# Kernel tuning notes

Hardware: AMD Instinct MI355X
Metric: run time of the kernel (lower is better)

The kernel has to match this reference:

```python
import jax, jax.numpy as jnp
import numpy as np

B, T, H, V = 32, 16, 768, 32000
EPS = 1e-5


def _conv(x, w, stride, pad):
    return jax.lax.conv_general_dilated(
        x, w, (stride, stride), [(pad, pad), (pad, pad)],
        dimension_numbers=('NCHW', 'OIHW', 'NCHW'))


def _bn(x, g, b, m, v):
    inv = g / jnp.sqrt(v + EPS)
    return x * inv[None, :, None, None] + (b - m * inv)[None, :, None, None]


def setup_inputs() -> dict:
    key = jax.random.key(0)
    ks = iter(jax.random.split(key, 48))

    def rn(shape, s=0.02):
        return s * jax.random.normal(next(ks), shape, jnp.float32)

    def bn_params(c):
        g = 1.0 + 0.1 * jax.random.normal(next(ks), (c,), jnp.float32)
        b = 0.1 * jax.random.normal(next(ks), (c,), jnp.float32)
        m = 0.1 * jax.random.normal(next(ks), (c,), jnp.float32)
        v = jax.random.uniform(next(ks), (c,), jnp.float32, 0.5, 1.5)
        return g, b, m, v

    inp = {}
    inp['images'] = jax.random.normal(next(ks), (B, 3, 224, 224), jnp.float32)
    inp['captions'] = jax.random.randint(next(ks), (B, T), 0, V)

    inp['conv1_w'] = rn((64, 3, 7, 7))
    inp['bn1_g'], inp['bn1_b'], inp['bn1_m'], inp['bn1_v'] = bn_params(64)
    inp['conv2_w'] = rn((128, 64, 3, 3))
    inp['bn2_g'], inp['bn2_b'], inp['bn2_m'], inp['bn2_v'] = bn_params(128)
    inp['conv3_w'] = rn((256, 128, 3, 3))
    inp['bn3_g'], inp['bn3_b'], inp['bn3_m'], inp['bn3_v'] = bn_params(256)
    inp['conv4_w'] = rn((H, 256, 3, 3))
    inp['bn4_g'], inp['bn4_b'], inp['bn4_m'], inp['bn4_v'] = bn_params(H)

    emb = rn((V, H), 1.0)
    inp['emb_table'] = emb.at[0].set(0.0)  # padding_idx=0 row is zero
    inp['attn_w'] = rn((H, H))             # attn_proj (no bias)
    inp['w_ih'] = rn((4 * H, 2 * H))       # LSTM input weights (i,f,g,o)
    inp['w_hh'] = rn((4 * H, H))
    inp['b_ih'] = rn((4 * H,))
    inp['b_hh'] = rn((4 * H,))
    inp['fc_w'] = rn((V, H))
    inp['fc_b'] = rn((V,))
    return inp


def _forward(images, captions, conv1_w, bn1_g, bn1_b, bn1_m, bn1_v,
             conv2_w, bn2_g, bn2_b, bn2_m, bn2_v,
             conv3_w, bn3_g, bn3_b, bn3_m, bn3_v,
             conv4_w, bn4_g, bn4_b, bn4_m, bn4_v,
             emb_table, attn_w, w_ih, w_hh, b_ih, b_hh, fc_w, fc_b):
    # ---- ResNetEncoder ----
    x = jax.nn.relu(_bn(_conv(images, conv1_w, 2, 3), bn1_g, bn1_b, bn1_m, bn1_v))
    x = jax.lax.reduce_window(x, -jnp.inf, jax.lax.max, (1, 1, 3, 3), (1, 1, 2, 2),
                              ((0, 0), (0, 0), (1, 1), (1, 1)))
    x = jax.nn.relu(_bn(_conv(x, conv2_w, 1, 1), bn2_g, bn2_b, bn2_m, bn2_v))
    x = jax.nn.relu(_bn(_conv(x, conv3_w, 2, 1), bn3_g, bn3_b, bn3_m, bn3_v))
    x = jax.nn.relu(_bn(_conv(x, conv4_w, 1, 1), bn4_g, bn4_b, bn4_m, bn4_v))
    b, c, hh, ww = x.shape
    memory = x.reshape(b, c, hh * ww).transpose(0, 2, 1)[:, :196, :]  # [B,196,H]

    # ---- LSTMAttnDecoder ----
    emb = emb_table[captions]  # [B,T,H]
    h0 = jnp.zeros((b, H), jnp.float32)
    c0 = jnp.zeros((b, H), jnp.float32)

    def step(carry, e_t):
        h, cst = carry
        q = h @ attn_w.T                                    # [B,H]
        scores = jnp.einsum('bh,bmh->bm', q, memory)        # [B,196]
        ctx = jnp.einsum('bm,bmh->bh', jax.nn.softmax(scores, axis=-1), memory)
        xin = jnp.concatenate([e_t, ctx], axis=-1)          # [B,2H]
        gates = xin @ w_ih.T + b_ih + h @ w_hh.T + b_hh     # [B,4H]
        i, f, g, o = jnp.split(gates, 4, axis=-1)
        c_new = jax.nn.sigmoid(f) * cst + jax.nn.sigmoid(i) * jnp.tanh(g)
        h_new = jax.nn.sigmoid(o) * jnp.tanh(c_new)
        logits = h_new @ fc_w.T + fc_b                      # [B,V]
        return (h_new, c_new), logits

    (hT, cT), logits = jax.lax.scan(step, (h0, c0), emb.transpose(1, 0, 2))
    logits = logits.transpose(1, 0, 2)  # [B,T,V]
    return logits, (hT[None], cT[None])


def reference(images, captions, conv1_w, bn1_g, bn1_b, bn1_m, bn1_v,
              conv2_w, bn2_g, bn2_b, bn2_m, bn2_v,
              conv3_w, bn3_g, bn3_b, bn3_m, bn3_v,
              conv4_w, bn4_g, bn4_b, bn4_m, bn4_v,
              emb_table, attn_w, w_ih, w_hh, b_ih, b_hh, fc_w, fc_b):
    return _forward(images, captions, conv1_w, bn1_g, bn1_b, bn1_m, bn1_v,
                    conv2_w, bn2_g, bn2_b, bn2_m, bn2_v,
                    conv3_w, bn3_g, bn3_b, bn3_m, bn3_v,
                    conv4_w, bn4_g, bn4_b, bn4_m, bn4_v,
                    emb_table, attn_w, w_ih, w_hh, b_ih, b_hh, fc_w, fc_b)
```

## Files before the change

### kernel.cpp

```cpp
#include <hip/hip_runtime.h>
#include <math.h>

#define NB 32
#define NT 16
#define NH 768
#define NV 32000

typedef short bf16x8 __attribute__((ext_vector_type(8)));
typedef float floatx4 __attribute__((ext_vector_type(4)));
typedef unsigned short ushort_t;

__device__ __forceinline__ float bf2f(unsigned short h) {
    unsigned u = ((unsigned)h) << 16;
    return __builtin_bit_cast(float, u);
}
__device__ __forceinline__ unsigned short f2bf(float f) {
    unsigned u = __builtin_bit_cast(unsigned, f);
    u += 0x7fffu + ((u >> 16) & 1u);
    return (unsigned short)(u >> 16);
}
__device__ __forceinline__ float sigmoidf_(float x) { return 1.f / (1.f + expf(-x)); }

__global__ void bn_prep(const float* __restrict__ g, const float* __restrict__ b,
                        const float* __restrict__ m, const float* __restrict__ v,
                        float* __restrict__ scale, float* __restrict__ bias, int C) {
    int i = blockIdx.x * 256 + threadIdx.x;
    if (i < C) {
        float inv = g[i] * rsqrtf(v[i] + 1e-5f);
        scale[i] = inv;
        bias[i] = b[i] - m[i] * inv;
    }
}

__global__ __launch_bounds__(256) void zfill(unsigned long long* __restrict__ p, long long n) {
    long long i = (long long)blockIdx.x * 256 + threadIdx.x;
    if (i < n) p[i] = 0ULL;
}

__global__ __launch_bounds__(256) void cvt_packW_conv(const float* __restrict__ w, ushort_t* __restrict__ dst,
                                                      int CIN, int total) {
    int idx = blockIdx.x * 256 + threadIdx.x;
    if (idx >= total) return;
    int e = idx & 7, lane = (idx >> 3) & 63, j = (idx >> 9) & 3;
    int r = idx >> 11;
    int KQ = CIN >> 5;
    int kq = r % KQ; r /= KQ;
    int tap = r % 9; int nt = r / 9;
    int co = nt * 64 + j * 16 + (lane & 15);
    int ci = kq * 32 + (lane >> 4) * 8 + e;
    dst[idx] = f2bf(w[((size_t)co * CIN + ci) * 9 + tap]);
}

__global__ __launch_bounds__(256) void cvt_wcombP(const float* __restrict__ w_ih, const float* __restrict__ w_hh,
                                                  ushort_t* __restrict__ dst) {
    int idx = blockIdx.x * 256 + threadIdx.x;
    if (idx >= 3072 * 1536) return;
    int e = idx & 7, lane = (idx >> 3) & 63;
    int t = idx >> 9;
    int kq = t % 48, gg = t / 48;
    int g = gg & 3, bx = gg >> 2;
    int j = g * 768 + bx * 16 + (lane & 15);
    int k = kq * 32 + (lane >> 4) * 8 + e;
    float v = (k < NH) ? w_ih[(size_t)j * (2 * NH) + NH + k] : w_hh[(size_t)j * NH + (k - NH)];
    dst[idx] = f2bf(v);
}

__global__ __launch_bounds__(256) void cvt_wattnTP(const float* __restrict__ w, ushort_t* __restrict__ dst) {
    int idx = blockIdx.x * 256 + threadIdx.x;
    if (idx >= 768 * 768) return;
    int e = idx & 7, lane = (idx >> 3) & 63, j = (idx >> 9) & 3;
    int t = idx >> 11;
    int kq = t % 24, nt = t / 24;
    int n = nt * 64 + 16 * j + (lane & 15);
    int k = kq * 32 + (lane >> 4) * 8 + e;
    dst[idx] = f2bf(w[(size_t)k * 768 + n]);
}

__global__ __launch_bounds__(256) void cvt_pad(const float* __restrict__ src, ushort_t* __restrict__ dst) {
    int idx = blockIdx.x * 256 + threadIdx.x;
    if (idx >= 64 * 160) return;
    int co = idx / 160, k = idx % 160;
    dst[idx] = (k < 147) ? f2bf(src[co * 147 + k]) : (ushort_t)0;
}

__global__ __launch_bounds__(256) void im2col1(const float* __restrict__ img, ushort_t* __restrict__ A) {
    int idx = blockIdx.x * 256 + threadIdx.x;
    const int total = 121856 * 160;
    if (idx >= total) return;
    int k = idx % 160;
    int m = idx / 160;
    ushort_t v = 0;
    if (k < 147) {
        int b = m / 3808;
        int rm = m % 3808;
        int y = rm / 112, x = rm % 112;
        int ci = k / 49;
        int r = k % 49;
        int ky = r / 7, kx = r % 7;
        int iy = 2 * y - 3 + ky;
        int ix = 2 * x - 3 + kx;
        if ((unsigned)iy < 224u && (unsigned)ix < 224u)
            v = f2bf(img[((size_t)(b * 3 + ci) * 224 + iy) * 224 + ix]);
    }
    A[idx] = v;
}

__global__ __launch_bounds__(256) void conv1_gemm(
    const ushort_t* __restrict__ A, const ushort_t* __restrict__ Bw,
    const float* __restrict__ scale, const float* __restrict__ bias,
    ushort_t* __restrict__ out) {
    int lane = threadIdx.x & 63, w = threadIdx.x >> 6;
    int m0 = (blockIdx.x * 4 + w) * 64;
    int lr = lane & 15, kl = (lane >> 4) * 8;
    floatx4 acc[4][4];
    #pragma unroll
    for (int i = 0; i < 4; ++i)
        #pragma unroll
        for (int j = 0; j < 4; ++j) acc[i][j] = 0.f;
    #pragma unroll
    for (int k0 = 0; k0 < 160; k0 += 32) {
        bf16x8 a[4], bb[4];
        #pragma unroll
        for (int i = 0; i < 4; ++i) a[i] = *(const bf16x8*)(A + (size_t)(m0 + 16 * i + lr) * 160 + kl + k0);
        #pragma unroll
        for (int j = 0; j < 4; ++j) bb[j] = *(const bf16x8*)(Bw + (size_t)(16 * j + lr) * 160 + kl + k0);
        #pragma unroll
        for (int i = 0; i < 4; ++i)
            #pragma unroll
            for (int j = 0; j < 4; ++j)
                acc[i][j] = __builtin_amdgcn_mfma_f32_16x16x32_bf16(a[i], bb[j], acc[i][j], 0, 0, 0);
    }
    #pragma unroll
    for (int i = 0; i < 4; ++i) {
        #pragma unroll
        for (int r = 0; r < 4; ++r) {
            int m = m0 + 16 * i + (lane >> 4) * 4 + r;
            int b = m / 3808;
            int rm = m % 3808;
            int y = rm / 112, x = rm % 112;
            #pragma unroll
            for (int j = 0; j < 4; ++j) {
                int n = 16 * j + lr;
                float v = fmaxf(acc[i][j][r] * scale[n] + bias[n], 0.f);
                out[((size_t)(b * 34 + y) * 112 + x) * 64 + n] = f2bf(v);
            }
        }
    }
}

__global__ __launch_bounds__(256) void pool_kernel(const ushort_t* __restrict__ in,
                                                   ushort_t* __restrict__ hal2) {
    int idx = blockIdx.x * 256 + threadIdx.x;
    const int total = 32 * 17 * 56 * 8;
    if (idx >= total) return;
    int c8 = idx & 7;
    int rest = idx >> 3;
    int x = rest % 56; rest /= 56;
    int y = rest % 17; int b = rest / 17;
    float mx[8];
    #pragma unroll
    for (int j = 0; j < 8; ++j) mx[j] = -INFINITY;
    for (int dy = -1; dy <= 1; ++dy) {
        int iy = 2 * y + dy;
        if ((unsigned)iy >= 34u) continue;
        for (int dx = -1; dx <= 1; ++dx) {
            int ix = 2 * x + dx;
            if ((unsigned)ix >= 112u) continue;
            bf16x8 v = *(const bf16x8*)(in + (((size_t)(b * 34 + iy)) * 112 + ix) * 64 + c8 * 8);
            #pragma unroll
            for (int j = 0; j < 8; ++j) mx[j] = fmaxf(mx[j], bf2f((unsigned short)v[j]));
        }
    }
    bf16x8 o;
    #pragma unroll
    for (int j = 0; j < 8; ++j) o[j] = (short)f2bf(mx[j]);
    *(bf16x8*)(hal2 + (((size_t)(b * 19 + y + 1)) * 58 + (x + 1)) * 64 + c8 * 8) = o;
}

template <int CIN, int HH, int WH, int STRIDE, int HOUT, int WOUT, int COUT, int MEMOUT, int OH, int OW>
__global__ __launch_bounds__(64) void conv_mfma(
    const ushort_t* __restrict__ in, const ushort_t* __restrict__ wtP,
    const float* __restrict__ scale, const float* __restrict__ bias,
    ushort_t* __restrict__ out) {
    int lane = threadIdx.x;
    int mt = blockIdx.x, nt = blockIdx.y;
    int lr = lane & 15, kl = (lane >> 4) * 8;
    int rowoff[4];
    #pragma unroll
    for (int i = 0; i < 4; ++i) {
        int m = mt * 64 + 16 * i + lr;
        int b = m / (HOUT * WOUT);
        int rm = m % (HOUT * WOUT);
        int y = rm / WOUT, x = rm % WOUT;
        rowoff[i] = ((b * HH + y * STRIDE) * WH + x * STRIDE) * CIN + kl;
    }
    floatx4 acc[4][4];
    #pragma unroll
    for (int i = 0; i < 4; ++i)
        #pragma unroll
        for (int j = 0; j < 4; ++j) acc[i][j] = 0.f;

    #pragma unroll
    for (int ky = 0; ky < 3; ++ky) {
        #pragma unroll
        for (int kx = 0; kx < 3; ++kx) {
            int ioff = (ky * WH + kx) * CIN;
            int t = ky * 3 + kx;
            #pragma unroll
            for (int k0 = 0; k0 < CIN; k0 += 32) {
                bf16x8 a[4], bb[4];
                #pragma unroll
                for (int i = 0; i < 4; ++i)
                    a[i] = *(const bf16x8*)(in + rowoff[i] + ioff + k0);
                #pragma unroll
                for (int j = 0; j < 4; ++j)
                    bb[j] = *(const bf16x8*)(wtP + ((((size_t)(nt * 9 + t) * (CIN / 32) + (k0 >> 5)) * 4 + j) * 64 + lane) * 8);
                #pragma unroll
                for (int i = 0; i < 4; ++i)
                    #pragma unroll
                    for (int j = 0; j < 4; ++j)
                        acc[i][j] = __builtin_amdgcn_mfma_f32_16x16x32_bf16(a[i], bb[j], acc[i][j], 0, 0, 0);
            }
        }
    }
    #pragma unroll
    for (int i = 0; i < 4; ++i) {
        #pragma unroll
        for (int r = 0; r < 4; ++r) {
            int m = mt * 64 + 16 * i + (lane >> 4) * 4 + r;
            int b = m / (HOUT * WOUT);
            int rm = m % (HOUT * WOUT);
            int y = rm / WOUT, x = rm % WOUT;
            #pragma unroll
            for (int j = 0; j < 4; ++j) {
                int n = nt * 64 + 16 * j + lr;
                float v = fmaxf(acc[i][j][r] * scale[n] + bias[n], 0.f);
                ushort_t hv = f2bf(v);
                if (MEMOUT) {
                    out[(size_t)m * COUT + n] = hv;
                } else {
                    out[((size_t)(b * OH + y + 1) * OW + (x + 1)) * COUT + n] = hv;
                }
            }
        }
    }
}

__global__ __launch_bounds__(64) void kmat_gemm(
    const ushort_t* __restrict__ memv, const ushort_t* __restrict__ Bp,
    ushort_t* __restrict__ KT) {
    int lane = threadIdx.x;
    int mt = blockIdx.x, nt = blockIdx.y;
    int lr = lane & 15, kl = (lane >> 4) * 8;
    floatx4 acc[4][4];
    #pragma unroll
    for (int i = 0; i < 4; ++i)
        #pragma unroll
        for (int j = 0; j < 4; ++j) acc[i][j] = 0.f;
    for (int kq = 0; kq < 24; ++kq) {
        bf16x8 a[4], bb[4];
        #pragma unroll
        for (int i = 0; i < 4; ++i)
            a[i] = *(const bf16x8*)(memv + (size_t)(mt * 64 + 16 * i + lr) * 768 + kq * 32 + kl);
        #pragma unroll
        for (int j = 0; j < 4; ++j)
            bb[j] = *(const bf16x8*)(Bp + (((size_t)(nt * 24 + kq) * 4 + j) * 64 + lane) * 8);
        #pragma unroll
        for (int i = 0; i < 4; ++i)
            #pragma unroll
            for (int j = 0; j < 4; ++j)
                acc[i][j] = __builtin_amdgcn_mfma_f32_16x16x32_bf16(a[i], bb[j], acc[i][j], 0, 0, 0);
    }
    #pragma unroll
    for (int i = 0; i < 4; ++i) {
        #pragma unroll
        for (int r = 0; r < 4; ++r) {
            int mg = mt * 64 + 16 * i + (lane >> 4) * 4 + r;
            int b = mg / 196, m = mg % 196;
            #pragma unroll
            for (int j = 0; j < 4; ++j) {
                int n = nt * 64 + 16 * j + lr;
                KT[(((size_t)b * 96 + (n >> 3)) * 196 + m) * 8 + (n & 7)] = f2bf(acc[i][j][r]);
            }
        }
    }
}

__global__ __launch_bounds__(256) void gather_embP(const int* __restrict__ caps,
                                                   const float* __restrict__ table,
                                                   ushort_t* __restrict__ dst) {
    int idx = blockIdx.x * 256 + threadIdx.x;
    if (idx >= 512 * 768) return;
    int e = idx & 7, lane = (idx >> 3) & 63, i = (idx >> 9) & 3;
    int t2 = idx >> 11;
    int kq = t2 % 24, mt = t2 / 24;
    int r = mt * 64 + i * 16 + (lane & 15);
    int k = kq * 32 + (lane >> 4) * 8 + e;
    int t = r >> 5, b = r & 31;
    dst[idx] = f2bf(table[(size_t)caps[b * NT + t] * NH + k]);
}

template <int REMAP>
__global__ __launch_bounds__(256) void gemm_staged(
    const ushort_t* __restrict__ Ap, const float* __restrict__ B,
    const float* __restrict__ bias1, const float* __restrict__ bias2,
    float* __restrict__ C, int ldb, int N) {
    __shared__ ushort_t bl[12 * 2048];
    int tid = threadIdx.x;
    int lane = tid & 63, w = tid >> 6;
    int nt = blockIdx.x;
    int r = tid >> 2, c0 = (tid & 3) * 8;
    const float* bsrc = B + (size_t)(nt * 64 + r) * ldb + c0;
    ushort_t* wbase = bl + (((r >> 4) * 64 + ((r & 15) | ((tid & 3) << 4))) * 8);
    floatx4 acc[2][4][4];
    #pragma unroll
    for (int h = 0; h < 2; ++h)
        #pragma unroll
        for (int i = 0; i < 4; ++i)
            #pragma unroll
            for (int j = 0; j < 4; ++j) acc[h][i][j] = 0.f;

    bf16x8 v[12];
    #pragma unroll
    for (int kk = 0; kk < 12; ++kk) {
        const float* p = bsrc + (size_t)kk * 32;
        float4 x0 = *(const float4*)p, x1 = *(const float4*)(p + 4);
        bf16x8 t8;
        t8[0] = (short)f2bf(x0.x); t8[1] = (short)f2bf(x0.y);
        t8[2] = (short)f2bf(x0.z); t8[3] = (short)f2bf(x0.w);
        t8[4] = (short)f2bf(x1.x); t8[5] = (short)f2bf(x1.y);
        t8[6] = (short)f2bf(x1.z); t8[7] = (short)f2bf(x1.w);
        v[kk] = t8;
    }
    #pragma unroll
    for (int s = 0; s < 2; ++s) {
        if (s) __syncthreads();
        #pragma unroll
        for (int kk = 0; kk < 12; ++kk) *(bf16x8*)(wbase + kk * 2048) = v[kk];
        __syncthreads();
        if (s == 0) {
            #pragma unroll
            for (int kk = 0; kk < 12; ++kk) {
                const float* p = bsrc + (size_t)(12 + kk) * 32;
                float4 x0 = *(const float4*)p, x1 = *(const float4*)(p + 4);
                bf16x8 t8;
                t8[0] = (short)f2bf(x0.x); t8[1] = (short)f2bf(x0.y);
                t8[2] = (short)f2bf(x0.z); t8[3] = (short)f2bf(x0.w);
                t8[4] = (short)f2bf(x1.x); t8[5] = (short)f2bf(x1.y);
                t8[6] = (short)f2bf(x1.z); t8[7] = (short)f2bf(x1.w);
                v[kk] = t8;
            }
        }
        #pragma unroll
        for (int kk = 0; kk < 12; ++kk) {
            int kq = s * 12 + kk;
            bf16x8 bb[4];
            #pragma unroll
            for (int j = 0; j < 4; ++j) bb[j] = *(const bf16x8*)(bl + ((kk * 4 + j) * 64 + lane) * 8);
            #pragma unroll
            for (int h = 0; h < 2; ++h) {
                int mt = w + h * 4;
                bf16x8 a[4];
                #pragma unroll
                for (int i = 0; i < 4; ++i)
                    a[i] = *(const bf16x8*)(Ap + ((((size_t)mt * 24 + kq) * 4 + i) * 64 + lane) * 8);
                #pragma unroll
                for (int i = 0; i < 4; ++i)
                    #pragma unroll
                    for (int j = 0; j < 4; ++j)
                        acc[h][i][j] = __builtin_amdgcn_mfma_f32_16x16x32_bf16(a[i], bb[j], acc[h][i][j], 0, 0, 0);
            }
        }
    }
    int lr = lane & 15;
    #pragma unroll
    for (int h = 0; h < 2; ++h) {
        int mt = w + h * 4;
        #pragma unroll
        for (int i = 0; i < 4; ++i) {
            #pragma unroll
            for (int rr = 0; rr < 4; ++rr) {
                int m = mt * 64 + 16 * i + (lane >> 4) * 4 + rr;
                #pragma unroll
                for (int j = 0; j < 4; ++j) {
                    int n = nt * 64 + 16 * j + lr;
                    float vv = acc[h][i][j][rr];
                    if (bias1) vv += bias1[n];
                    if (bias2) vv += bias2[n];
                    if (REMAP) {
                        int t = m >> 5, b = m & 31;
                        C[(size_t)((b << 4) + t) * NV + n] = vv;
                    } else {
                        C[(size_t)m * N + n] = vv;
                    }
                }
            }
        }
    }
}

__global__ __launch_bounds__(768) void attn2(
    ushort_t* __restrict__ xin, const ushort_t* __restrict__ KT,
    const ushort_t* __restrict__ mem) {
    __shared__ float hq[NH];
    __shared__ float sl[196];
    __shared__ float red[16];
    int b = blockIdx.x, tid = threadIdx.x;
    hq[tid] = bf2f(xin[(size_t)b * 1536 + NH + tid]);
    __syncthreads();
    if (tid < 392) {
        int m = tid >> 1, half = tid & 1;
        const ushort_t* basep = KT + (((size_t)b * 96 + half * 48) * 196 + m) * 8;
        float acc = 0.f;
        #pragma unroll 4
        for (int k8 = 0; k8 < 48; ++k8) {
            bf16x8 v = *(const bf16x8*)(basep + (size_t)k8 * 196 * 8);
            const float* qp = hq + (half * 48 + k8) * 8;
            #pragma unroll
            for (int j = 0; j < 8; ++j)
                acc = fmaf(bf2f((unsigned short)v[j]), qp[j], acc);
        }
        acc += __shfl_xor(acc, 1);
        if (!half) sl[m] = acc;
    }
    __syncthreads();
    float sc = (tid < 196) ? sl[tid] : -INFINITY;
    float v = sc;
    #pragma unroll
    for (int off = 32; off; off >>= 1) v = fmaxf(v, __shfl_down(v, off));
    if ((tid & 63) == 0) red[tid >> 6] = v;
    __syncthreads();
    if (tid == 0) {
        float m = red[0];
        for (int i = 1; i < 12; ++i) m = fmaxf(m, red[i]);
        red[12] = m;
    }
    __syncthreads();
    float mx = red[12];
    float e = (tid < 196) ? expf(sc - mx) : 0.f;
    __syncthreads();
    v = e;
    #pragma unroll
    for (int off = 32; off; off >>= 1) v += __shfl_down(v, off);
    if ((tid & 63) == 0) red[tid >> 6] = v;
    __syncthreads();
    if (tid == 0) {
        float s = red[0];
        for (int i = 1; i < 12; ++i) s += red[i];
        red[12] = 1.f / s;
    }
    __syncthreads();
    if (tid < 196) sl[tid] = e * red[12];
    __syncthreads();
    {
        float acc = 0.f;
        const ushort_t* mb = mem + (size_t)b * 196 * NH + tid;
        #pragma unroll 4
        for (int m = 0; m < 196; ++m) acc = fmaf(sl[m], bf2f(mb[(size_t)m * NH]), acc);
        xin[(size_t)b * 1536 + tid] = f2bf(acc);
    }
}

__global__ __launch_bounds__(256) void step_fused(
    const ushort_t* __restrict__ xin_r, const ushort_t* __restrict__ wcombP,
    const float* __restrict__ eg_t,
    float* __restrict__ cbuf, float* __restrict__ hbuf,
    ushort_t* __restrict__ xin_w, ushort_t* __restrict__ hallP, int tstep) {
    __shared__ float pbuf[4][64][33];
    int lane = threadIdx.x & 63, w = threadIdx.x >> 6;
    int bx = blockIdx.x;
    int lr = lane & 15, kl = (lane >> 4) * 8;
    floatx4 acc[2][4];
    #pragma unroll
    for (int i = 0; i < 2; ++i)
        #pragma unroll
        for (int g = 0; g < 4; ++g) acc[i][g] = 0.f;
    for (int kq = 0; kq < 12; ++kq) {
        int k = w * 384 + kq * 32;
        bf16x8 a[2], bb[4];
        #pragma unroll
        for (int i = 0; i < 2; ++i)
            a[i] = *(const bf16x8*)(xin_r + (size_t)(16 * i + lr) * 1536 + k + kl);
        #pragma unroll
        for (int g = 0; g < 4; ++g)
            bb[g] = *(const bf16x8*)(wcombP + (((size_t)(bx * 4 + g) * 48 + (w * 12 + kq)) * 64 + lane) * 8);
        #pragma unroll
        for (int i = 0; i < 2; ++i)
            #pragma unroll
            for (int g = 0; g < 4; ++g)
                acc[i][g] = __builtin_amdgcn_mfma_f32_16x16x32_bf16(a[i], bb[g], acc[i][g], 0, 0, 0);
    }
    #pragma unroll
    for (int i = 0; i < 2; ++i)
        #pragma unroll
        for (int g = 0; g < 4; ++g)
            #pragma unroll
            for (int r = 0; r < 4; ++r) {
                int m = 16 * i + (lane >> 4) * 4 + r;
                pbuf[w][g * 16 + lr][m] = acc[i][g][r];
            }
    __syncthreads();
    int tid = threadIdx.x;
    #pragma unroll
    for (int o = 0; o < 2; ++o) {
        int pid = tid * 2 + o;
        int m = pid & 31, c = pid >> 5;
        int kcol = bx * 16 + c;
        float gi = 0.f, gf = 0.f, gg = 0.f, go = 0.f;
        #pragma unroll
        for (int ww = 0; ww < 4; ++ww) {
            gi += pbuf[ww][c][m];
            gf += pbuf[ww][16 + c][m];
            gg += pbuf[ww][32 + c][m];
            go += pbuf[ww][48 + c][m];
        }
        const float* eg = eg_t + (size_t)m * 3072;
        gi += eg[kcol];
        gf += eg[768 + kcol];
        gg += eg[1536 + kcol];
        go += eg[2304 + kcol];
        float cst = cbuf[m * 768 + kcol];
        float cn = sigmoidf_(gf) * cst + sigmoidf_(gi) * tanhf(gg);
        float hn = sigmoidf_(go) * tanhf(cn);
        cbuf[m * 768 + kcol] = cn;
        hbuf[m * 768 + kcol] = hn;
        ushort_t hb = f2bf(hn);
        xin_w[(size_t)m * 1536 + NH + kcol] = hb;
        int rrow = tstep * 32 + m;
        int mtp = rrow >> 6, ip = (rrow >> 4) & 3, lrp = rrow & 15;
        int kqp = kcol >> 5, hip = (kcol >> 3) & 3, ep = kcol & 7;
        hallP[((((size_t)mtp * 24 + kqp) * 4 + ip) * 64 + (lrp | (hip << 4))) * 8 + ep] = hb;
    }
}

__global__ __launch_bounds__(256) void zero_state(float* __restrict__ h, float* __restrict__ c,
                                                  ushort_t* __restrict__ xin) {
    int i = blockIdx.x * 256 + threadIdx.x;
    if (i < NB * 1536) xin[i] = 0;
    if (i < NB * NH) { h[i] = 0.f; c[i] = 0.f; }
}

__global__ __launch_bounds__(256) void copy_hc(const float* __restrict__ h, const float* __restrict__ c,
                                               float* __restrict__ out) {
    int i = blockIdx.x * 256 + threadIdx.x;
    if (i < NB * NH) {
        out[(size_t)NB * NT * NV + i] = h[i];
        out[(size_t)NB * NT * NV + NB * NH + i] = c[i];
    }
}

extern "C" void kernel_launch(void* const* d_in, const int* in_sizes, int n_in,
                              void* d_out, int out_size, void* d_ws, size_t ws_size,
                              hipStream_t stream) {
    const float* images   = (const float*)d_in[0];
    const int*   captions = (const int*)d_in[1];
    const float* conv1_w  = (const float*)d_in[2];
    const float* bn1_g = (const float*)d_in[3], *bn1_b = (const float*)d_in[4];
    const float* bn1_m = (const float*)d_in[5], *bn1_v = (const float*)d_in[6];
    const float* conv2_w  = (const float*)d_in[7];
    const float* bn2_g = (const float*)d_in[8], *bn2_b = (const float*)d_in[9];
    const float* bn2_m = (const float*)d_in[10], *bn2_v = (const float*)d_in[11];
    const float* conv3_w  = (const float*)d_in[12];
    const float* bn3_g = (const float*)d_in[13], *bn3_b = (const float*)d_in[14];
    const float* bn3_m = (const float*)d_in[15], *bn3_v = (const float*)d_in[16];
    const float* conv4_w  = (const float*)d_in[17];
    const float* bn4_g = (const float*)d_in[18], *bn4_b = (const float*)d_in[19];
    const float* bn4_m = (const float*)d_in[20], *bn4_v = (const float*)d_in[21];
    const float* emb_table = (const float*)d_in[22];
    const float* attn_w   = (const float*)d_in[23];
    const float* w_ih     = (const float*)d_in[24];
    const float* w_hh     = (const float*)d_in[25];
    const float* b_ih     = (const float*)d_in[26];
    const float* b_hh     = (const float*)d_in[27];
    const float* fc_w     = (const float*)d_in[28];
    const float* fc_b     = (const float*)d_in[29];
    float* out = (float*)d_out;

    char* base = (char*)d_ws;
    size_t off = 0;
    auto alloc = [&](size_t bytes) { char* p = base + off; off += (bytes + 255) & ~(size_t)255; return p; };
    float* s1 = (float*)alloc(64 * 4);   float* bb1 = (float*)alloc(64 * 4);
    float* s2 = (float*)alloc(128 * 4);  float* bb2 = (float*)alloc(128 * 4);
    float* s3 = (float*)alloc(256 * 4);  float* bb3 = (float*)alloc(256 * 4);
    float* s4 = (float*)alloc(768 * 4);  float* bb4 = (float*)alloc(768 * 4);
    ushort_t* c1out = (ushort_t*)alloc((size_t)32 * 34 * 112 * 64 * 2);
    size_t halo_start = off;
    ushort_t* hal2 = (ushort_t*)alloc((size_t)32 * 19 * 58 * 64 * 2);
    ushort_t* hal3 = (ushort_t*)alloc((size_t)32 * 18 * 58 * 128 * 2);
    ushort_t* hal4 = (ushort_t*)alloc((size_t)32 * 10 * 30 * 256 * 2);
    size_t halo_bytes = off - halo_start;
    ushort_t* memv = (ushort_t*)alloc((size_t)32 * 196 * 768 * 2);
    ushort_t* KT   = (ushort_t*)alloc((size_t)32 * 96 * 196 * 8 * 2);
    ushort_t* wb1 = (ushort_t*)alloc((size_t)64 * 160 * 2);
    ushort_t* wb2 = (ushort_t*)alloc((size_t)128 * 9 * 64 * 2);
    ushort_t* wb3 = (ushort_t*)alloc((size_t)256 * 9 * 128 * 2);
    ushort_t* wb4 = (ushort_t*)alloc((size_t)768 * 9 * 256 * 2);
    ushort_t* wattnTP = (ushort_t*)alloc((size_t)768 * 768 * 2);
    ushort_t* wcombP = (ushort_t*)alloc((size_t)3072 * 1536 * 2);
    ushort_t* e512P = (ushort_t*)alloc((size_t)512 * 768 * 2);
    float* eg   = (float*)alloc((size_t)512 * 3072 * 4);
    ushort_t* HallP = (ushort_t*)alloc((size_t)512 * 768 * 2);
    float* hbuf = (float*)alloc(NB * NH * 4);
    float* cbuf = (float*)alloc(NB * NH * 4);
    ushort_t* xinA = (ushort_t*)alloc((size_t)NB * 1536 * 2);
    ushort_t* xinB = (ushort_t*)alloc((size_t)NB * 1536 * 2);
    ushort_t* imcol = (ushort_t*)alloc((size_t)121856 * 160 * 2);

    bn_prep<<<1, 256, 0, stream>>>(bn1_g, bn1_b, bn1_m, bn1_v, s1, bb1, 64);
    bn_prep<<<1, 256, 0, stream>>>(bn2_g, bn2_b, bn2_m, bn2_v, s2, bb2, 128);
    bn_prep<<<1, 256, 0, stream>>>(bn3_g, bn3_b, bn3_m, bn3_v, s3, bb3, 256);
    bn_prep<<<3, 256, 0, stream>>>(bn4_g, bn4_b, bn4_m, bn4_v, s4, bb4, 768);
    cvt_pad<<<(64 * 160 + 255) / 256, 256, 0, stream>>>(conv1_w, wb1);
    cvt_packW_conv<<<(128 * 9 * 64 + 255) / 256, 256, 0, stream>>>(conv2_w, wb2, 64, 128 * 9 * 64);
    cvt_packW_conv<<<(256 * 9 * 128 + 255) / 256, 256, 0, stream>>>(conv3_w, wb3, 128, 256 * 9 * 128);
    cvt_packW_conv<<<(768 * 9 * 256 + 255) / 256, 256, 0, stream>>>(conv4_w, wb4, 256, 768 * 9 * 256);
    cvt_wattnTP<<<(768 * 768 + 255) / 256, 256, 0, stream>>>(attn_w, wattnTP);
    cvt_wcombP<<<(3072 * 1536 + 255) / 256, 256, 0, stream>>>(w_ih, w_hh, wcombP);
    {
        long long n8 = (long long)(halo_bytes / 8);
        zfill<<<(unsigned)((n8 + 255) / 256), 256, 0, stream>>>((unsigned long long*)hal2, n8);
    }

    im2col1<<<(121856 * 160 + 255) / 256, 256, 0, stream>>>(images, imcol);
    conv1_gemm<<<476, 256, 0, stream>>>(imcol, wb1, s1, bb1, c1out);
    pool_kernel<<<(32 * 17 * 56 * 8 + 255) / 256, 256, 0, stream>>>(c1out, hal2);
    conv_mfma<64, 19, 58, 1, 16, 56, 128, 0, 18, 58>
        <<<dim3(448, 2), 64, 0, stream>>>(hal2, wb2, s2, bb2, hal3);
    conv_mfma<128, 18, 58, 2, 8, 28, 256, 0, 10, 30>
        <<<dim3(112, 4), 64, 0, stream>>>(hal3, wb3, s3, bb3, hal4);
    conv_mfma<256, 10, 30, 1, 7, 28, 768, 1, 1, 1>
        <<<dim3(98, 12), 64, 0, stream>>>(hal4, wb4, s4, bb4, memv);

    kmat_gemm<<<dim3(98, 12), 64, 0, stream>>>(memv, wattnTP, KT);

    gather_embP<<<(512 * 768) / 256, 256, 0, stream>>>(captions, emb_table, e512P);
    gemm_staged<0><<<48, 256, 0, stream>>>(e512P, w_ih, b_ih, b_hh, eg, 2 * NH, 3072);
    zero_state<<<(NB * 1536 + 255) / 256, 256, 0, stream>>>(hbuf, cbuf, xinA);

    ushort_t* xcur = xinA;
    ushort_t* xnxt = xinB;
    for (int t = 0; t < NT; ++t) {
        attn2<<<NB, NH, 0, stream>>>(xcur, KT, memv);
        step_fused<<<48, 256, 0, stream>>>(
            xcur, wcombP, eg + (size_t)t * NB * 3072, cbuf, hbuf, xnxt, HallP, t);
        ushort_t* tmp = xcur; xcur = xnxt; xnxt = tmp;
    }

    gemm_staged<1><<<500, 256, 0, stream>>>(HallP, fc_w, fc_b, nullptr, out, NH, NV);

    copy_hc<<<(NB * NH + 255) / 256, 256, 0, stream>>>(hbuf, cbuf, out);
}
```

Baseline: 958.7 us.

## Double-buffer B tiles in staged GEMM and merge BN prep launches

```diff
diff --git a/kernel.cpp b/kernel.cpp
--- a/kernel.cpp
+++ b/kernel.cpp
@@ -21,15 +21,34 @@
 }
 __device__ __forceinline__ float sigmoidf_(float x) { return 1.f / (1.f + expf(-x)); }
 
-__global__ void bn_prep(const float* __restrict__ g, const float* __restrict__ b,
-                        const float* __restrict__ m, const float* __restrict__ v,
-                        float* __restrict__ scale, float* __restrict__ bias, int C) {
+__device__ __forceinline__ bf16x8 cvt8(float4 a, float4 b) {
+    bf16x8 t;
+    t[0] = (short)f2bf(a.x); t[1] = (short)f2bf(a.y);
+    t[2] = (short)f2bf(a.z); t[3] = (short)f2bf(a.w);
+    t[4] = (short)f2bf(b.x); t[5] = (short)f2bf(b.y);
+    t[6] = (short)f2bf(b.z); t[7] = (short)f2bf(b.w);
+    return t;
+}
+
+__global__ __launch_bounds__(256) void bn_prep4(
+    const float* __restrict__ g1, const float* __restrict__ b1, const float* __restrict__ m1, const float* __restrict__ v1,
+    const float* __restrict__ g2, const float* __restrict__ b2, const float* __restrict__ m2, const float* __restrict__ v2,
+    const float* __restrict__ g3, const float* __restrict__ b3, const float* __restrict__ m3, const float* __restrict__ v3,
+    const float* __restrict__ g4, const float* __restrict__ b4, const float* __restrict__ m4, const float* __restrict__ v4,
+    float* __restrict__ s1, float* __restrict__ o1, float* __restrict__ s2, float* __restrict__ o2,
+    float* __restrict__ s3, float* __restrict__ o3, float* __restrict__ s4, float* __restrict__ o4) {
     int i = blockIdx.x * 256 + threadIdx.x;
-    if (i < C) {
-        float inv = g[i] * rsqrtf(v[i] + 1e-5f);
-        scale[i] = inv;
-        bias[i] = b[i] - m[i] * inv;
-    }
+    const float *g, *b, *m, *v;
+    float *s, *o;
+    int c;
+    if (i < 64)        { g = g1; b = b1; m = m1; v = v1; s = s1; o = o1; c = i; }
+    else if (i < 192)  { g = g2; b = b2; m = m2; v = v2; s = s2; o = o2; c = i - 64; }
+    else if (i < 448)  { g = g3; b = b3; m = m3; v = v3; s = s3; o = o3; c = i - 192; }
+    else if (i < 1216) { g = g4; b = b4; m = m4; v = v4; s = s4; o = o4; c = i - 448; }
+    else return;
+    float inv = g[c] * rsqrtf(v[c] + 1e-5f);
+    s[c] = inv;
+    o[c] = b[c] - m[c] * inv;
 }
 
 __global__ __launch_bounds__(256) void zfill(unsigned long long* __restrict__ p, long long n) {
@@ -301,17 +320,19 @@
 }
 
 template <int REMAP>
-__global__ __launch_bounds__(256) void gemm_staged(
+__global__ __launch_bounds__(256) void gemm_pipe(
     const ushort_t* __restrict__ Ap, const float* __restrict__ B,
     const float* __restrict__ bias1, const float* __restrict__ bias2,
     float* __restrict__ C, int ldb, int N) {
-    __shared__ ushort_t bl[12 * 2048];
+    __shared__ ushort_t bl[2][2048];
     int tid = threadIdx.x;
     int lane = tid & 63, w = tid >> 6;
     int nt = blockIdx.x;
     int r = tid >> 2, c0 = (tid & 3) * 8;
     const float* bsrc = B + (size_t)(nt * 64 + r) * ldb + c0;
-    ushort_t* wbase = bl + (((r >> 4) * 64 + ((r & 15) | ((tid & 3) << 4))) * 8);
+    int slotoff = (((r >> 4) * 64 + ((r & 15) | ((tid & 3) << 4))) * 8);
+    ushort_t* slot0 = &bl[0][0] + slotoff;
+    ushort_t* slot1 = &bl[1][0] + slotoff;
     floatx4 acc[2][4][4];
     #pragma unroll
     for (int h = 0; h < 2; ++h)
@@ -320,56 +341,38 @@
             #pragma unroll
             for (int j = 0; j < 4; ++j) acc[h][i][j] = 0.f;
 
-    bf16x8 v[12];
-    #pragma unroll
-    for (int kk = 0; kk < 12; ++kk) {
-        const float* p = bsrc + (size_t)kk * 32;
-        float4 x0 = *(const float4*)p, x1 = *(const float4*)(p + 4);
-        bf16x8 t8;
-        t8[0] = (short)f2bf(x0.x); t8[1] = (short)f2bf(x0.y);
-        t8[2] = (short)f2bf(x0.z); t8[3] = (short)f2bf(x0.w);
-        t8[4] = (short)f2bf(x1.x); t8[5] = (short)f2bf(x1.y);
-        t8[6] = (short)f2bf(x1.z); t8[7] = (short)f2bf(x1.w);
-        v[kk] = t8;
-    }
-    #pragma unroll
-    for (int s = 0; s < 2; ++s) {
-        if (s) __syncthreads();
-        #pragma unroll
-        for (int kk = 0; kk < 12; ++kk) *(bf16x8*)(wbase + kk * 2048) = v[kk];
+    float4 p0a = *(const float4*)(bsrc),      p0b = *(const float4*)(bsrc + 4);
+    float4 fa0 = *(const float4*)(bsrc + 32), fa1 = *(const float4*)(bsrc + 36);
+    float4 fb0 = *(const float4*)(bsrc + 64), fb1 = *(const float4*)(bsrc + 68);
+    *(bf16x8*)slot0 = cvt8(p0a, p0b);
+
+    for (int j = 0; j < 24; ++j) {
         __syncthreads();
-        if (s == 0) {
-            #pragma unroll
-            for (int kk = 0; kk < 12; ++kk) {
-                const float* p = bsrc + (size_t)(12 + kk) * 32;
-                float4 x0 = *(const float4*)p, x1 = *(const float4*)(p + 4);
-                bf16x8 t8;
-                t8[0] = (short)f2bf(x0.x); t8[1] = (short)f2bf(x0.y);
-                t8[2] = (short)f2bf(x0.z); t8[3] = (short)f2bf(x0.w);
-                t8[4] = (short)f2bf(x1.x); t8[5] = (short)f2bf(x1.y);
-                t8[6] = (short)f2bf(x1.z); t8[7] = (short)f2bf(x1.w);
-                v[kk] = t8;
-            }
-        }
-        #pragma unroll
-        for (int kk = 0; kk < 12; ++kk) {
-            int kq = s * 12 + kk;
-            bf16x8 bb[4];
-            #pragma unroll
-            for (int j = 0; j < 4; ++j) bb[j] = *(const bf16x8*)(bl + ((kk * 4 + j) * 64 + lane) * 8);
-            #pragma unroll
-            for (int h = 0; h < 2; ++h) {
-                int mt = w + h * 4;
-                bf16x8 a[4];
+        if (j < 23) {
+            *(bf16x8*)((j & 1) ? slot0 : slot1) = cvt8(fa0, fa1);
+            fa0 = fb0; fa1 = fb1;
+        }
+        if (j < 21) {
+            const float* p = bsrc + (size_t)(j + 3) * 32;
+            fb0 = *(const float4*)p;
+            fb1 = *(const float4*)(p + 4);
+        }
+        const ushort_t* rb = &bl[j & 1][0];
+        bf16x8 bb[4];
+        #pragma unroll
+        for (int j4 = 0; j4 < 4; ++j4) bb[j4] = *(const bf16x8*)(rb + (j4 * 64 + lane) * 8);
+        #pragma unroll
+        for (int h = 0; h < 2; ++h) {
+            int mt = w + h * 4;
+            bf16x8 a[4];
+            #pragma unroll
+            for (int i = 0; i < 4; ++i)
+                a[i] = *(const bf16x8*)(Ap + ((((size_t)mt * 24 + j) * 4 + i) * 64 + lane) * 8);
+            #pragma unroll
+            for (int i = 0; i < 4; ++i)
                 #pragma unroll
-                for (int i = 0; i < 4; ++i)
-                    a[i] = *(const bf16x8*)(Ap + ((((size_t)mt * 24 + kq) * 4 + i) * 64 + lane) * 8);
-                #pragma unroll
-                for (int i = 0; i < 4; ++i)
-                    #pragma unroll
-                    for (int j = 0; j < 4; ++j)
-                        acc[h][i][j] = __builtin_amdgcn_mfma_f32_16x16x32_bf16(a[i], bb[j], acc[h][i][j], 0, 0, 0);
-            }
+                for (int j4 = 0; j4 < 4; ++j4)
+                    acc[h][i][j4] = __builtin_amdgcn_mfma_f32_16x16x32_bf16(a[i], bb[j4], acc[h][i][j4], 0, 0, 0);
         }
     }
     int lr = lane & 15;
@@ -382,9 +385,9 @@
             for (int rr = 0; rr < 4; ++rr) {
                 int m = mt * 64 + 16 * i + (lane >> 4) * 4 + rr;
                 #pragma unroll
-                for (int j = 0; j < 4; ++j) {
-                    int n = nt * 64 + 16 * j + lr;
-                    float vv = acc[h][i][j][rr];
+                for (int j4 = 0; j4 < 4; ++j4) {
+                    int n = nt * 64 + 16 * j4 + lr;
+                    float vv = acc[h][i][j4][rr];
                     if (bias1) vv += bias1[n];
                     if (bias2) vv += bias2[n];
                     if (REMAP) {
@@ -606,10 +609,11 @@
     ushort_t* xinB = (ushort_t*)alloc((size_t)NB * 1536 * 2);
     ushort_t* imcol = (ushort_t*)alloc((size_t)121856 * 160 * 2);
 
-    bn_prep<<<1, 256, 0, stream>>>(bn1_g, bn1_b, bn1_m, bn1_v, s1, bb1, 64);
-    bn_prep<<<1, 256, 0, stream>>>(bn2_g, bn2_b, bn2_m, bn2_v, s2, bb2, 128);
-    bn_prep<<<1, 256, 0, stream>>>(bn3_g, bn3_b, bn3_m, bn3_v, s3, bb3, 256);
-    bn_prep<<<3, 256, 0, stream>>>(bn4_g, bn4_b, bn4_m, bn4_v, s4, bb4, 768);
+    bn_prep4<<<5, 256, 0, stream>>>(bn1_g, bn1_b, bn1_m, bn1_v,
+                                    bn2_g, bn2_b, bn2_m, bn2_v,
+                                    bn3_g, bn3_b, bn3_m, bn3_v,
+                                    bn4_g, bn4_b, bn4_m, bn4_v,
+                                    s1, bb1, s2, bb2, s3, bb3, s4, bb4);
     cvt_pad<<<(64 * 160 + 255) / 256, 256, 0, stream>>>(conv1_w, wb1);
     cvt_packW_conv<<<(128 * 9 * 64 + 255) / 256, 256, 0, stream>>>(conv2_w, wb2, 64, 128 * 9 * 64);
     cvt_packW_conv<<<(256 * 9 * 128 + 255) / 256, 256, 0, stream>>>(conv3_w, wb3, 128, 256 * 9 * 128);
@@ -634,7 +638,7 @@
     kmat_gemm<<<dim3(98, 12), 64, 0, stream>>>(memv, wattnTP, KT);
 
     gather_embP<<<(512 * 768) / 256, 256, 0, stream>>>(captions, emb_table, e512P);
-    gemm_staged<0><<<48, 256, 0, stream>>>(e512P, w_ih, b_ih, b_hh, eg, 2 * NH, 3072);
+    gemm_pipe<0><<<48, 256, 0, stream>>>(e512P, w_ih, b_ih, b_hh, eg, 2 * NH, 3072);
     zero_state<<<(NB * 1536 + 255) / 256, 256, 0, stream>>>(hbuf, cbuf, xinA);
 
     ushort_t* xcur = xinA;
@@ -646,7 +650,7 @@
         ushort_t* tmp = xcur; xcur = xnxt; xnxt = tmp;
     }
 
-    gemm_staged<1><<<500, 256, 0, stream>>>(HallP, fc_w, fc_b, nullptr, out, NH, NV);
+    gemm_pipe<1><<<500, 256, 0, stream>>>(HallP, fc_w, fc_b, nullptr, out, NH, NV);
 
     copy_hc<<<(NB * NH + 255) / 256, 256, 0, stream>>>(hbuf, cbuf, out);
 }
```

Result: faster. 923.3 us (-3.7%).
